# Performance work log

Hardware: AMD Instinct MI355X
Metric: run time of the kernel (lower is better)

## Reference

```python
import jax, jax.numpy as jnp
import numpy as np

N = 100000       # nodes
E = 1600000      # edges (avg degree 16)
IN_DIM = 128
HIDDEN = 128


def _glorot(key, shape):
    s = 1.0 / np.sqrt(shape[0])
    return jax.random.uniform(key, shape, minval=-s, maxval=s, dtype=jnp.float32)


def setup_inputs() -> dict:
    key = jax.random.key(0)
    ks = jax.random.split(key, 8)
    x = jax.random.normal(ks[0], (N, IN_DIM), dtype=jnp.float32)
    edge_index = jax.random.randint(ks[1], (2, E), 0, N, dtype=jnp.int32)
    W0 = _glorot(ks[2], (IN_DIM, HIDDEN))
    b0 = jnp.zeros((HIDDEN,), dtype=jnp.float32)
    W1 = _glorot(ks[3], (HIDDEN, HIDDEN))
    b1 = jnp.zeros((HIDDEN,), dtype=jnp.float32)
    W2 = _glorot(ks[4], (HIDDEN, HIDDEN))
    b2 = jnp.zeros((HIDDEN,), dtype=jnp.float32)
    return {"x": x, "edge_index": edge_index,
            "W0": W0, "b0": b0, "W1": W1, "b1": b1, "W2": W2, "b2": b2}


def _gcn_conv(x, row, col, norm, W, b):
    # x' = W x, then out[i] = sum_{j in N(i) U {i}} norm_ji * x'[j], + bias
    h = x @ W                              # [N, out]
    msg = norm[:, None] * h[row]           # [E+N, out] gather + scale
    out = jax.ops.segment_sum(msg, col, num_segments=N)  # scatter-add
    return out + b


def reference(x, edge_index, W0, b0, W1, b1, W2, b2):
    # PyG GCNConv default: add self-loops, symmetric normalization D^-1/2 A D^-1/2
    self_loops = jnp.arange(N, dtype=edge_index.dtype)
    row = jnp.concatenate([edge_index[0], self_loops])  # sources
    col = jnp.concatenate([edge_index[1], self_loops])  # destinations
    deg = jax.ops.segment_sum(jnp.ones_like(col, dtype=x.dtype), col, num_segments=N)
    dinv = jax.lax.rsqrt(deg)              # deg >= 1 thanks to self-loops
    norm = dinv[row] * dinv[col]           # [E+N]

    h = _gcn_conv(x, row, col, norm, W0, b0)
    h = jax.nn.relu(h)                     # dropout: eval mode (identity)
    h = _gcn_conv(h, row, col, norm, W1, b1)
    h = jax.nn.relu(h)
    return _gcn_conv(h, row, col, norm, W2, b2)
```

## Files before the change

kernel.cpp:

```cpp
#include <hip/hip_runtime.h>

#define HID 128
#define BR  128
#define FILL_CHUNK 2048

typedef _Float16 f16;
typedef f16 f16x2 __attribute__((ext_vector_type(2)));
typedef f16 f16x4 __attribute__((ext_vector_type(4)));
typedef f16 f16x8 __attribute__((ext_vector_type(8)));
typedef float f32x4 __attribute__((ext_vector_type(4)));

static __device__ __forceinline__ float2 h2f(unsigned int u) {
    f16x2 v;
    __builtin_memcpy(&v, &u, 4);
    return make_float2((float)v[0], (float)v[1]);
}


__global__ void k_prep_count(const float* __restrict__ W0, const float* __restrict__ W1,
                             const float* __restrict__ W2, f16* __restrict__ wt,
                             const int* __restrict__ col, int* __restrict__ cnt8,
                             int E, int N) {
    if (blockIdx.x < 48) {
        const int b = blockIdx.x;
        const int which = b >> 4;
        const float* W = which == 0 ? W0 : (which == 1 ? W1 : W2);
        f16* o = wt + which * 32768;
        int i = (b & 15) * 256 + threadIdx.x;
        int k = i >> 5, n0 = (i & 31) * 4;
        float4 v = reinterpret_cast<const float4*>(W)[i];
        float vv[4] = {v.x, v.y, v.z, v.w};
#pragma unroll
        for (int e = 0; e < 4; ++e) {
            int n = n0 + e;
            int idx = (k >> 3) * 1024 + n * 8 + (k & 7);
            f16 h = (f16)vv[e];
            o[idx] = h;
            o[16384 + idx] = (f16)(vv[e] - (float)h);
        }
    } else {
        const int bb = blockIdx.x - 48;
        int* cnt = cnt8 + (size_t)(bb & 7) * N;
        const int eend = min(E, (bb + 1) * FILL_CHUNK);
        for (int e = bb * FILL_CHUNK + threadIdx.x; e < eend; e += 256)
            atomicAdd(&cnt[__builtin_nontemporal_load(col + e)], 1);
    }
}

__global__ void k_scan_block(const int* __restrict__ cnt8, int* __restrict__ excl,
                             int* __restrict__ bsum, float* __restrict__ dinv, int N) {
    __shared__ int s[256];
    int i = blockIdx.x * 256 + threadIdx.x;
    int v = 0;
    if (i < N) {
#pragma unroll
        for (int x = 0; x < 8; ++x) v += cnt8[(size_t)x * N + i];
        dinv[i] = 1.0f / sqrtf((float)(v + 1));
    }
    s[threadIdx.x] = v;
    __syncthreads();
    for (int off = 1; off < 256; off <<= 1) {
        int t = (threadIdx.x >= off) ? s[threadIdx.x - off] : 0;
        __syncthreads();
        s[threadIdx.x] += t;
        __syncthreads();
    }
    if (i < N) excl[i] = s[threadIdx.x] - v;
    if (threadIdx.x == 255) bsum[blockIdx.x] = s[255];
}

__global__ __launch_bounds__(1024) void k_scan_bsum(int* __restrict__ bsum, int nb) {
    __shared__ int s[1024];
    int i = threadIdx.x;
    int v = (i < nb) ? bsum[i] : 0;
    s[i] = v;
    __syncthreads();
    for (int off = 1; off < 1024; off <<= 1) {
        int t = (i >= off) ? s[i - off] : 0;
        __syncthreads();
        s[i] += t;
        __syncthreads();
    }
    if (i < nb) bsum[i] = s[i] - v;
}

__global__ void k_scan_add(int* __restrict__ row_ptr, const int* __restrict__ bsum,
                           int* __restrict__ fill, int N, int E) {
    int i = blockIdx.x * 256 + threadIdx.x;
    if (i < N) {
        int v = row_ptr[i] + bsum[blockIdx.x];
        row_ptr[i] = v;
        fill[i] = v;
    }
    if (i == 0) row_ptr[N] = E;
}

__global__ void k_fill(const int* __restrict__ row, const int* __restrict__ col,
                       int* __restrict__ fill, int* __restrict__ csr_src, int E, int N) {
    const int win = blockIdx.x & 3;
    const int chunk = blockIdx.x >> 2;
    const int per = (N + 3) >> 2;
    const int lo = win * per;
    const int hi = min(N, lo + per);
    const int eend = min(E, (chunk + 1) * FILL_CHUNK);
    for (int e = chunk * FILL_CHUNK + threadIdx.x; e < eend; e += 256) {
        int c = col[e];
        if (c >= lo && c < hi) {
            int p = atomicAdd(&fill[c], 1);
            csr_src[p] = row[e];
        }
    }
}


template<int MODE>
__global__ __launch_bounds__(512, 4) void k_gemm(const void* __restrict__ Xv,
                                                 const f16* __restrict__ Wt,
                                                 const float* __restrict__ dinv,
                                                 f16* __restrict__ H, int N) {
    __shared__ f16 Xs[16384];
    const int t = threadIdx.x;
    const int row0 = blockIdx.x * BR;

    const int w  = t >> 6;
    const int l  = t & 63;
    const int lg = l >> 4;
    const int li = l & 15;
    const int ng = w & 3;
    const int mg = w >> 2;

    f16x8 Wh[2][4], Wl[2][4];
#pragma unroll
    for (int nb = 0; nb < 2; ++nb) {
        const int ncol = (ng * 2 + nb) * 16 + li;
#pragma unroll
        for (int ks = 0; ks < 4; ++ks) {
            const int idx = (ks * 4 + lg) * 1024 + ncol * 8;
            Wh[nb][ks] = *reinterpret_cast<const f16x8*>(&Wt[idx]);
            Wl[nb][ks] = *reinterpret_cast<const f16x8*>(&Wt[16384 + idx]);
        }
    }

    if constexpr (MODE == 0) {
        const float* X = (const float*)Xv;
        for (int i = t; i < 4096; i += 512) {
            int r = i >> 5, q = i & 31;
            int gr = row0 + r;
            float4 v = make_float4(0.f, 0.f, 0.f, 0.f);
            if (gr < N) v = reinterpret_cast<const float4*>(X + (size_t)gr * HID)[q];
            int base = r * 128 + (((q >> 1) ^ (r & 7)) * 8) + (q & 1) * 4;
            *reinterpret_cast<f16x4*>(&Xs[base]) =
                (f16x4){(f16)v.x, (f16)v.y, (f16)v.z, (f16)v.w};
        }
    } else {
        const f16* src = (const f16*)Xv + (size_t)row0 * HID;
        for (int i = t; i < 2048; i += 512)
            *reinterpret_cast<f16x8*>(&Xs[i * 8]) = *reinterpret_cast<const f16x8*>(src + (size_t)i * 8);
    }
    __syncthreads();

    f32x4 acc[2][4];
#pragma unroll
    for (int nb = 0; nb < 2; ++nb)
#pragma unroll
        for (int mb = 0; mb < 4; ++mb) acc[nb][mb] = (f32x4){0.f, 0.f, 0.f, 0.f};

#pragma unroll
    for (int mb = 0; mb < 4; ++mb) {
        const int arow = mg * 64 + mb * 16 + li;
#pragma unroll
        for (int ks = 0; ks < 4; ++ks) {
            const int idx = arow * 128 + (((ks * 4 + lg) ^ (arow & 7)) * 8);
            f16x8 Xh = *reinterpret_cast<const f16x8*>(&Xs[idx]);
#pragma unroll
            for (int nb = 0; nb < 2; ++nb) {
                acc[nb][mb] = __builtin_amdgcn_mfma_f32_16x16x32_f16(Wh[nb][ks], Xh, acc[nb][mb], 0, 0, 0);
                acc[nb][mb] = __builtin_amdgcn_mfma_f32_16x16x32_f16(Wl[nb][ks], Xh, acc[nb][mb], 0, 0, 0);
            }
        }
    }

#pragma unroll
    for (int mb = 0; mb < 4; ++mb) {
        const int m = row0 + mg * 64 + mb * 16 + li;
        if (m < N) {
            const float d = dinv[m];
#pragma unroll
            for (int nb = 0; nb < 2; ++nb) {
                f16x4 o = {(f16)(acc[nb][mb][0] * d), (f16)(acc[nb][mb][1] * d),
                           (f16)(acc[nb][mb][2] * d), (f16)(acc[nb][mb][3] * d)};
                *reinterpret_cast<f16x4*>(&H[(size_t)m * HID + (ng * 2 + nb) * 16 + lg * 4]) = o;
            }
        }
    }
}


template<bool F16OUT>
__global__ __launch_bounds__(256) void k_agg_csr(const f16* __restrict__ h,
                                                 const int* __restrict__ csr_src,
                                                 const int* __restrict__ row_ptr,
                                                 const float* __restrict__ dinv,
                                                 const float* __restrict__ bias,
                                                 void* __restrict__ outv, int N) {
    const int node = blockIdx.x * 8 + (threadIdx.x >> 5);
    if (node >= N) return;
    const int l = threadIdx.x & 31;
    const uint2* h2 = reinterpret_cast<const uint2*>(h);

    uint2 us = h2[(size_t)node * 32 + l];
    float2 a0 = h2f(us.x), a1 = h2f(us.y);
    float acc0 = a0.x, acc1 = a0.y, acc2 = a1.x, acc3 = a1.y;

    int j = row_ptr[node];
    const int end = row_ptr[node + 1];

    int s0, s1, s2, s3, s4, s5, s6, s7;
    bool have = (j + 8 <= end);
    if (have) {
        s0 = csr_src[j];     s1 = csr_src[j + 1];
        s2 = csr_src[j + 2]; s3 = csr_src[j + 3];
        s4 = csr_src[j + 4]; s5 = csr_src[j + 5];
        s6 = csr_src[j + 6]; s7 = csr_src[j + 7];
    }
    while (have) {
        const int jn = j + 8;
        const bool haven = (jn + 8 <= end);
        int t0, t1, t2, t3, t4, t5, t6, t7;
        if (haven) {
            t0 = csr_src[jn];     t1 = csr_src[jn + 1];
            t2 = csr_src[jn + 2]; t3 = csr_src[jn + 3];
            t4 = csr_src[jn + 4]; t5 = csr_src[jn + 5];
            t6 = csr_src[jn + 6]; t7 = csr_src[jn + 7];
        }
        uint2 u0 = h2[(size_t)s0 * 32 + l];
        uint2 u1 = h2[(size_t)s1 * 32 + l];
        uint2 u2 = h2[(size_t)s2 * 32 + l];
        uint2 u3 = h2[(size_t)s3 * 32 + l];
        uint2 u4 = h2[(size_t)s4 * 32 + l];
        uint2 u5 = h2[(size_t)s5 * 32 + l];
        uint2 u6 = h2[(size_t)s6 * 32 + l];
        uint2 u7 = h2[(size_t)s7 * 32 + l];
        float2 v0 = h2f(u0.x), w0 = h2f(u0.y), v1 = h2f(u1.x), w1 = h2f(u1.y);
        float2 v2 = h2f(u2.x), w2 = h2f(u2.y), v3 = h2f(u3.x), w3 = h2f(u3.y);
        float2 v4 = h2f(u4.x), w4 = h2f(u4.y), v5 = h2f(u5.x), w5 = h2f(u5.y);
        float2 v6 = h2f(u6.x), w6 = h2f(u6.y), v7 = h2f(u7.x), w7 = h2f(u7.y);
        acc0 += ((v0.x + v1.x) + (v2.x + v3.x)) + ((v4.x + v5.x) + (v6.x + v7.x));
        acc1 += ((v0.y + v1.y) + (v2.y + v3.y)) + ((v4.y + v5.y) + (v6.y + v7.y));
        acc2 += ((w0.x + w1.x) + (w2.x + w3.x)) + ((w4.x + w5.x) + (w6.x + w7.x));
        acc3 += ((w0.y + w1.y) + (w2.y + w3.y)) + ((w4.y + w5.y) + (w6.y + w7.y));
        s0 = t0; s1 = t1; s2 = t2; s3 = t3; s4 = t4; s5 = t5; s6 = t6; s7 = t7;
        j = jn;
        have = haven;
    }
    for (; j < end; ++j) {
        uint2 u = h2[(size_t)csr_src[j] * 32 + l];
        float2 v = h2f(u.x), w = h2f(u.y);
        acc0 += v.x; acc1 += v.y; acc2 += w.x; acc3 += w.y;
    }

    const float di = dinv[node];
    const float4 bv = reinterpret_cast<const float4*>(bias)[l];
    float o0 = fmaf(di, acc0, bv.x);
    float o1 = fmaf(di, acc1, bv.y);
    float o2 = fmaf(di, acc2, bv.z);
    float o3 = fmaf(di, acc3, bv.w);

    if constexpr (F16OUT) {
        o0 = fmaxf(o0, 0.f); o1 = fmaxf(o1, 0.f);
        o2 = fmaxf(o2, 0.f); o3 = fmaxf(o3, 0.f);
        const int swz = (((l >> 1) ^ (node & 7)) << 1) | (l & 1);
        f16x4 o = {(f16)o0, (f16)o1, (f16)o2, (f16)o3};
        *reinterpret_cast<f16x4*>((f16*)outv + (size_t)node * HID + swz * 4) = o;
    } else {
        *reinterpret_cast<float4*>((float*)outv + (size_t)node * HID + l * 4) =
            make_float4(o0, o1, o2, o3);
    }
}


extern "C" void kernel_launch(void* const* d_in, const int* in_sizes, int n_in,
                              void* d_out, int out_size, void* d_ws, size_t ws_size,
                              hipStream_t stream) {
    const float* x  = (const float*)d_in[0];
    const int*   ei = (const int*)  d_in[1];
    const float* W0 = (const float*)d_in[2];
    const float* b0 = (const float*)d_in[3];
    const float* W1 = (const float*)d_in[4];
    const float* b1 = (const float*)d_in[5];
    const float* W2 = (const float*)d_in[6];
    const float* b2 = (const float*)d_in[7];

    const int N = in_sizes[0] / HID;
    const int E = in_sizes[1] / 2;
    const int* row = ei;
    const int* col = ei + E;

    const int nb_n = (N + 255) / 256;

    f16*   h16     = (f16*)d_ws;
    float* dinv    = (float*)(h16 + (size_t)N * HID);
    int*   cnt8    = (int*)(dinv + N);
    int*   row_ptr = cnt8 + (size_t)8 * N;
    int*   fill    = row_ptr + (N + 1);
    int*   bsum    = fill + N;
    int*   csr_src = bsum + nb_n;
    f16*   wt      = (f16*)(csr_src + E);
    f16*   wt0     = wt;
    f16*   wt1     = wt + 32768;
    f16*   wt2     = wt + 65536;
    f16*   act     = (f16*)d_out;
    float* out     = (float*)d_out;

    const int nb_gemm  = (N + BR - 1) / BR;
    const int nb_agg   = (N + 7) / 8;
    const int nb_chunk = (E + FILL_CHUNK - 1) / FILL_CHUNK;
    const int nb_fill  = nb_chunk * 4;

    (void)hipMemsetAsync(cnt8, 0, (size_t)8 * N * sizeof(int), stream);
    k_prep_count<<<nb_chunk + 48, 256, 0, stream>>>(W0, W1, W2, wt, col, cnt8, E, N);
    k_scan_block<<<nb_n, 256, 0, stream>>>(cnt8, row_ptr, bsum, dinv, N);
    k_scan_bsum <<<1, 1024, 0, stream>>>(bsum, nb_n);
    k_scan_add  <<<nb_n, 256, 0, stream>>>(row_ptr, bsum, fill, N, E);
    k_fill      <<<nb_fill, 256, 0, stream>>>(row, col, fill, csr_src, E, N);

    k_gemm<0>      <<<nb_gemm, 512, 0, stream>>>(x, wt0, dinv, h16, N);
    k_agg_csr<true><<<nb_agg, 256, 0, stream>>>(h16, csr_src, row_ptr, dinv, b0, act, N);
    k_gemm<1>      <<<nb_gemm, 512, 0, stream>>>(act, wt1, dinv, h16, N);
    k_agg_csr<true><<<nb_agg, 256, 0, stream>>>(h16, csr_src, row_ptr, dinv, b1, act, N);
    k_gemm<1>      <<<nb_gemm, 512, 0, stream>>>(act, wt2, dinv, h16, N);
    k_agg_csr<false><<<nb_agg, 256, 0, stream>>>(h16, csr_src, row_ptr, dinv, b2, out, N);
}
```

Measured before the change: 412.1 us.

## Fuse CSR fill into first GEMM launch as extra blocks and split by XCD windows

The CSR fill pass now runs as extra blocks appended to the layer-0 GEMM launch, so the independent fill and GEMM work can overlap on the GPU instead of running back to back. The fill partition changes from 4 to 8 destination windows, with block index low bits choosing the window, likely so each XCD's atomics hit a disjoint node range. Fill blocks now use 512 threads and carry the GEMM kernel's shared memory allocation, which may lower their occupancy. The templated GEMM is split into two separate kernels.

Result: no change. 418.7 us (+1.6%).

```diff
diff --git a/kernel.cpp b/kernel.cpp
--- a/kernel.cpp
+++ b/kernel.cpp
@@ -95,30 +95,36 @@
     if (i == 0) row_ptr[N] = E;
 }
 
-__global__ void k_fill(const int* __restrict__ row, const int* __restrict__ col,
-                       int* __restrict__ fill, int* __restrict__ csr_src, int E, int N) {
-    const int win = blockIdx.x & 3;
-    const int chunk = blockIdx.x >> 2;
-    const int per = (N + 3) >> 2;
-    const int lo = win * per;
-    const int hi = min(N, lo + per);
-    const int eend = min(E, (chunk + 1) * FILL_CHUNK);
-    for (int e = chunk * FILL_CHUNK + threadIdx.x; e < eend; e += 256) {
-        int c = col[e];
-        if (c >= lo && c < hi) {
-            int p = atomicAdd(&fill[c], 1);
-            csr_src[p] = row[e];
-        }
-    }
-}
-
-
-template<int MODE>
-__global__ __launch_bounds__(512, 4) void k_gemm(const void* __restrict__ Xv,
-                                                 const f16* __restrict__ Wt,
-                                                 const float* __restrict__ dinv,
-                                                 f16* __restrict__ H, int N) {
+
+__global__ __launch_bounds__(512, 4) void k_gemm0_fill(const float* __restrict__ X,
+                                                       const f16* __restrict__ Wt,
+                                                       const float* __restrict__ dinv,
+                                                       f16* __restrict__ H, int N,
+                                                       const int* __restrict__ row,
+                                                       const int* __restrict__ col,
+                                                       int* __restrict__ fill,
+                                                       int* __restrict__ csr_src,
+                                                       int E, int nb_gemm) {
     __shared__ f16 Xs[16384];
+
+    if ((int)blockIdx.x >= nb_gemm) {
+        const int fb = blockIdx.x - nb_gemm;
+        const int xcd = fb & 7;
+        const int chunk = fb >> 3;
+        const int per = (N + 7) >> 3;
+        const int lo = xcd * per;
+        const int hi = min(N, lo + per);
+        const int eend = min(E, (chunk + 1) * FILL_CHUNK);
+        for (int e = chunk * FILL_CHUNK + threadIdx.x; e < eend; e += 512) {
+            int c = col[e];
+            if (c >= lo && c < hi) {
+                int p = atomicAdd(&fill[c], 1);
+                csr_src[p] = row[e];
+            }
+        }
+        return;
+    }
+
     const int t = threadIdx.x;
     const int row0 = blockIdx.x * BR;
 
@@ -141,22 +147,84 @@
         }
     }
 
-    if constexpr (MODE == 0) {
-        const float* X = (const float*)Xv;
-        for (int i = t; i < 4096; i += 512) {
-            int r = i >> 5, q = i & 31;
-            int gr = row0 + r;
-            float4 v = make_float4(0.f, 0.f, 0.f, 0.f);
-            if (gr < N) v = reinterpret_cast<const float4*>(X + (size_t)gr * HID)[q];
-            int base = r * 128 + (((q >> 1) ^ (r & 7)) * 8) + (q & 1) * 4;
-            *reinterpret_cast<f16x4*>(&Xs[base]) =
-                (f16x4){(f16)v.x, (f16)v.y, (f16)v.z, (f16)v.w};
-        }
-    } else {
-        const f16* src = (const f16*)Xv + (size_t)row0 * HID;
-        for (int i = t; i < 2048; i += 512)
-            *reinterpret_cast<f16x8*>(&Xs[i * 8]) = *reinterpret_cast<const f16x8*>(src + (size_t)i * 8);
-    }
+    for (int i = t; i < 4096; i += 512) {
+        int r = i >> 5, q = i & 31;
+        int gr = row0 + r;
+        float4 v = make_float4(0.f, 0.f, 0.f, 0.f);
+        if (gr < N) v = reinterpret_cast<const float4*>(X + (size_t)gr * HID)[q];
+        int base = r * 128 + (((q >> 1) ^ (r & 7)) * 8) + (q & 1) * 4;
+        *reinterpret_cast<f16x4*>(&Xs[base]) =
+            (f16x4){(f16)v.x, (f16)v.y, (f16)v.z, (f16)v.w};
+    }
+    __syncthreads();
+
+    f32x4 acc[2][4];
+#pragma unroll
+    for (int nb = 0; nb < 2; ++nb)
+#pragma unroll
+        for (int mb = 0; mb < 4; ++mb) acc[nb][mb] = (f32x4){0.f, 0.f, 0.f, 0.f};
+
+#pragma unroll
+    for (int mb = 0; mb < 4; ++mb) {
+        const int arow = mg * 64 + mb * 16 + li;
+#pragma unroll
+        for (int ks = 0; ks < 4; ++ks) {
+            const int idx = arow * 128 + (((ks * 4 + lg) ^ (arow & 7)) * 8);
+            f16x8 Xh = *reinterpret_cast<const f16x8*>(&Xs[idx]);
+#pragma unroll
+            for (int nb = 0; nb < 2; ++nb) {
+                acc[nb][mb] = __builtin_amdgcn_mfma_f32_16x16x32_f16(Wh[nb][ks], Xh, acc[nb][mb], 0, 0, 0);
+                acc[nb][mb] = __builtin_amdgcn_mfma_f32_16x16x32_f16(Wl[nb][ks], Xh, acc[nb][mb], 0, 0, 0);
+            }
+        }
+    }
+
+#pragma unroll
+    for (int mb = 0; mb < 4; ++mb) {
+        const int m = row0 + mg * 64 + mb * 16 + li;
+        if (m < N) {
+            const float d = dinv[m];
+#pragma unroll
+            for (int nb = 0; nb < 2; ++nb) {
+                f16x4 o = {(f16)(acc[nb][mb][0] * d), (f16)(acc[nb][mb][1] * d),
+                           (f16)(acc[nb][mb][2] * d), (f16)(acc[nb][mb][3] * d)};
+                *reinterpret_cast<f16x4*>(&H[(size_t)m * HID + (ng * 2 + nb) * 16 + lg * 4]) = o;
+            }
+        }
+    }
+}
+
+
+__global__ __launch_bounds__(512, 4) void k_gemm1(const f16* __restrict__ Xv,
+                                                  const f16* __restrict__ Wt,
+                                                  const float* __restrict__ dinv,
+                                                  f16* __restrict__ H, int N) {
+    __shared__ f16 Xs[16384];
+    const int t = threadIdx.x;
+    const int row0 = blockIdx.x * BR;
+
+    const int w  = t >> 6;
+    const int l  = t & 63;
+    const int lg = l >> 4;
+    const int li = l & 15;
+    const int ng = w & 3;
+    const int mg = w >> 2;
+
+    f16x8 Wh[2][4], Wl[2][4];
+#pragma unroll
+    for (int nb = 0; nb < 2; ++nb) {
+        const int ncol = (ng * 2 + nb) * 16 + li;
+#pragma unroll
+        for (int ks = 0; ks < 4; ++ks) {
+            const int idx = (ks * 4 + lg) * 1024 + ncol * 8;
+            Wh[nb][ks] = *reinterpret_cast<const f16x8*>(&Wt[idx]);
+            Wl[nb][ks] = *reinterpret_cast<const f16x8*>(&Wt[16384 + idx]);
+        }
+    }
+
+    const f16* src = Xv + (size_t)row0 * HID;
+    for (int i = t; i < 2048; i += 512)
+        *reinterpret_cast<f16x8*>(&Xs[i * 8]) = *reinterpret_cast<const f16x8*>(src + (size_t)i * 8);
     __syncthreads();
 
     f32x4 acc[2][4];
@@ -315,19 +383,19 @@
     const int nb_gemm  = (N + BR - 1) / BR;
     const int nb_agg   = (N + 7) / 8;
     const int nb_chunk = (E + FILL_CHUNK - 1) / FILL_CHUNK;
-    const int nb_fill  = nb_chunk * 4;
+    const int nb_fill  = nb_chunk * 8;
 
     (void)hipMemsetAsync(cnt8, 0, (size_t)8 * N * sizeof(int), stream);
     k_prep_count<<<nb_chunk + 48, 256, 0, stream>>>(W0, W1, W2, wt, col, cnt8, E, N);
     k_scan_block<<<nb_n, 256, 0, stream>>>(cnt8, row_ptr, bsum, dinv, N);
     k_scan_bsum <<<1, 1024, 0, stream>>>(bsum, nb_n);
     k_scan_add  <<<nb_n, 256, 0, stream>>>(row_ptr, bsum, fill, N, E);
-    k_fill      <<<nb_fill, 256, 0, stream>>>(row, col, fill, csr_src, E, N);
-
-    k_gemm<0>      <<<nb_gemm, 512, 0, stream>>>(x, wt0, dinv, h16, N);
+
+    k_gemm0_fill<<<nb_gemm + nb_fill, 512, 0, stream>>>(x, wt0, dinv, h16, N,
+                                                        row, col, fill, csr_src, E, nb_gemm);
     k_agg_csr<true><<<nb_agg, 256, 0, stream>>>(h16, csr_src, row_ptr, dinv, b0, act, N);
-    k_gemm<1>      <<<nb_gemm, 512, 0, stream>>>(act, wt1, dinv, h16, N);
+    k_gemm1<<<nb_gemm, 512, 0, stream>>>(act, wt1, dinv, h16, N);
     k_agg_csr<true><<<nb_agg, 256, 0, stream>>>(h16, csr_src, row_ptr, dinv, b1, act, N);
-    k_gemm<1>      <<<nb_gemm, 512, 0, stream>>>(act, wt2, dinv, h16, N);
+    k_gemm1<<<nb_gemm, 512, 0, stream>>>(act, wt2, dinv, h16, N);
     k_agg_csr<false><<<nb_agg, 256, 0, stream>>>(h16, csr_src, row_ptr, dinv, b2, out, N);
 }
```
